# Performance work log

Hardware: AMD Instinct MI355X
Metric: run time of the kernel (lower is better)

## Reference

```python
import jax, jax.numpy as jnp
import numpy as np

N_WIRES = 4
DIM = 16  # 2**4 state-vector length; wire 0 = most significant bit


def _ry(state, theta, wire):
    """Apply RY(theta) on `wire`. state: (N,16) real; theta: (N,) or scalar."""
    s = jnp.moveaxis(state.reshape(-1, 2, 2, 2, 2), 1 + wire, 1)
    c = jnp.cos(theta * 0.5)
    sn = jnp.sin(theta * 0.5)
    if jnp.ndim(theta):
        c = c.reshape(-1, 1, 1, 1)
        sn = sn.reshape(-1, 1, 1, 1)
    s0, s1 = s[:, 0], s[:, 1]
    out = jnp.stack([c * s0 - sn * s1, sn * s0 + c * s1], axis=1)
    return jnp.moveaxis(out, 1, 1 + wire).reshape(-1, DIM)


def _cx_perm(control, target):
    idx = np.arange(DIM)
    cbit = (idx >> (N_WIRES - 1 - control)) & 1
    return np.where(cbit == 1, idx ^ (1 << (N_WIRES - 1 - target)), idx)

# Pauli-Z expectation signs per wire: (16, 4)
_Z_SIGNS = np.stack(
    [1.0 - 2.0 * ((np.arange(DIM) >> (N_WIRES - 1 - w)) & 1) for w in range(N_WIRES)],
    axis=1,
).astype(np.float32)
_CX01 = _cx_perm(0, 1); _CX12 = _cx_perm(1, 2); _CX23 = _cx_perm(2, 3)
_CX02 = _cx_perm(0, 2); _CX13 = _cx_perm(1, 3)


def _init_state(n, dtype):
    return jnp.zeros((n, DIM), dtype).at[:, 0].set(1.0)  # |0000>


def _encode(angles):
    """Fresh device + RY(angle_w) on each wire. angles: (N,4) -> state (N,16)."""
    state = _init_state(angles.shape[0], angles.dtype)
    for w in range(N_WIRES):
        state = _ry(state, angles[:, w], w)
    return state


def _measure_z(state):
    return (state * state) @ jnp.asarray(_Z_SIGNS, state.dtype)  # (N,4)


def _quanv_features(angles, rl_params):
    """Encoder + fixed 8-op 'random layer' (5 RY + 3 CX) + MeasureAll(Z)."""
    s = _encode(angles)
    s = _ry(s, rl_params[0], 0)
    s = _ry(s, rl_params[1], 1)
    s = s[:, _CX02]
    s = _ry(s, rl_params[2], 2)
    s = _ry(s, rl_params[3], 3)
    s = s[:, _CX13]
    s = _ry(s, rl_params[4], 0)
    s = s[:, _CX23]
    return _measure_z(s)  # (N,4)


def _attn_raw(angles):
    """Encoder + CX(0,1),CX(1,2),CX(2,3), measure Z on wire 0."""
    s = _encode(angles)
    s = s[:, _CX01]
    s = s[:, _CX12]
    s = s[:, _CX23]
    return _measure_z(s)[:, 0]  # (N,)


def setup_inputs() -> dict:
    key = jax.random.key(0)
    k1, k2, k3 = jax.random.split(key, 3)
    B = 4096
    x = jax.random.uniform(k1, (B, 784), dtype=jnp.float32)
    rl_params = jax.random.normal(k2, (5,), dtype=jnp.float32)
    W = jax.random.normal(k3, (10, 784), dtype=jnp.float32) * 0.03
    b = jnp.zeros((10,), jnp.float32)
    return {"x": x, "rl_params": rl_params, "W": W, "b": b}


def reference(x, rl_params, W, b):
    B = x.shape[0]
    img = x.reshape(B, 28, 28)
    # 2x2 patches in row-major order -> (B*196, 4) with order [tl, tr, bl, br]
    angles = img.reshape(B, 14, 2, 14, 2).transpose(0, 1, 3, 2, 4).reshape(B * 196, 4)
    feats = _quanv_features(angles, rl_params).reshape(B, 196, 4)
    raw = _attn_raw(feats.reshape(B * 196, 4)).reshape(B, 196)
    attn = jax.nn.softmax(raw, axis=1)
    weighted = (feats * attn[:, :, None]).reshape(B, 4 * 14 * 14)
    logits = weighted @ W.T + b
    return jax.nn.log_softmax(logits, axis=-1)
```

## Files before the change

### kernel.cpp

```cpp
#include <hip/hip_runtime.h>

#define NTHREADS 256
#define NPATCH 196


__device__ __forceinline__ float dot4(float4 a, float4 b) {
    return a.x * b.x + a.y * b.y + a.z * b.z + a.w * b.w;
}

__device__ __forceinline__ float wave_sum63(float x) {
#define DPP_STEP(ctrl, rmask)                                                   \
    x += __int_as_float(__builtin_amdgcn_update_dpp(                            \
        0, __float_as_int(x), (ctrl), (rmask), 0xf, true));
    DPP_STEP(0x111, 0xf)
    DPP_STEP(0x112, 0xf)
    DPP_STEP(0x114, 0xf)
    DPP_STEP(0x118, 0xf)
    DPP_STEP(0x142, 0xa)
    DPP_STEP(0x143, 0xc)
#undef DPP_STEP
    return x;
}

__global__ __launch_bounds__(NTHREADS, 6) void quanv_fused(
    const float* __restrict__ x, const float* __restrict__ rl,
    const float* __restrict__ W, const float* __restrict__ bias,
    float* __restrict__ out)
{
    __shared__ float redw[4];
    __shared__ float redl[4][10];

    const int lane = threadIdx.x & 63;
    const int wave = threadIdx.x >> 6;
    const int il   = wave >> 1;
    const int half = wave & 1;
    const int img  = blockIdx.x * 2 + il;

    const float* __restrict__ xb = x + (size_t)img * 784;

    float srl2, crl2, srl4, crl4;
    __sincosf(rl[2], &srl2, &crl2);
    __sincosf(rl[4], &srl4, &crl4);
    const float rl0 = rl[0], rl1 = rl[1], rl3v = rl[3];

    const int p0 = half * 98 + lane;
    const bool has2 = (lane < 34);
    const int pp1 = has2 ? (p0 + 64) : p0;

    auto patchf = [&](int p, float& f0, float& f1, float& f2, float& f3) {
        const int pi = p / 14;
        const int base = 56 * pi + 2 * (p - pi * 14);
        const float2 top = *reinterpret_cast<const float2*>(xb + base);
        const float2 bot = *reinterpret_cast<const float2*>(xb + base + 28);
        float sa, ca; __sincosf(top.x + rl0, &sa, &ca);
        float s2, c2; __sincosf(bot.x, &s2, &c2);
        f1 = __cosf(top.y + rl1);
        const float cd = __cosf(bot.y + rl3v);
        f0 = crl4 * ca - srl4 * sa * s2;
        f2 = crl2 * ca * c2 - srl2 * s2;
        f3 = f1 * cd * f2;
    };

    float f00, f01, f02, f03; patchf(p0,  f00, f01, f02, f03);
    float f10, f11, f12, f13; patchf(pp1, f10, f11, f12, f13);

    const float e0 = __expf(__cosf(f00));
    const float e1 = has2 ? __expf(__cosf(f10)) : 0.f;

    const float svw = wave_sum63(e0 + e1);
    if (lane == 63) redw[wave] = svw;
    __syncthreads();
    const float inv = 1.0f / (redw[wave & ~1] + redw[wave | 1]);

    const float sc0 = e0 * inv, sc1 = e1 * inv;
    const float4 g0 = make_float4(f00 * sc0, f01 * sc0, f02 * sc0, f03 * sc0);
    const float4 g1 = make_float4(f10 * sc1, f11 * sc1, f12 * sc1, f13 * sc1);

    const float4* __restrict__ W4 = reinterpret_cast<const float4*>(W);
    float acc[10];
    #pragma unroll
    for (int k = 0; k < 10; ++k) {
        acc[k] = dot4(g0, W4[k * NPATCH + p0]) + dot4(g1, W4[k * NPATCH + pp1]);
    }

    #pragma unroll
    for (int k = 0; k < 10; ++k) acc[k] = wave_sum63(acc[k]);
    if (lane == 63) {
        #pragma unroll
        for (int k = 0; k < 10; ++k) redl[wave][k] = acc[k];
    }
    __syncthreads();

    if (half == 0) {
        float lg[10];
        #pragma unroll
        for (int k = 0; k < 10; ++k)
            lg[k] = redl[wave][k] + redl[wave + 1][k] + bias[k];
        float m2 = lg[0];
        #pragma unroll
        for (int k = 1; k < 10; ++k) m2 = fmaxf(m2, lg[k]);
        float ssum = 0.f;
        #pragma unroll
        for (int k = 0; k < 10; ++k) ssum += __expf(lg[k] - m2);
        const float lse = m2 + __logf(ssum);
        if (lane < 10) {
            float myv = lg[0];
            #pragma unroll
            for (int k = 1; k < 10; ++k) myv = (lane == k) ? lg[k] : myv;
            out[(size_t)img * 10 + lane] = myv - lse;
        }
    }
}

extern "C" void kernel_launch(void* const* d_in, const int* in_sizes, int n_in,
                              void* d_out, int out_size, void* d_ws, size_t ws_size,
                              hipStream_t stream) {
    const float* x    = (const float*)d_in[0];
    const float* rl   = (const float*)d_in[1];
    const float* W    = (const float*)d_in[2];
    const float* bias = (const float*)d_in[3];
    float* out = (float*)d_out;
    const int B = in_sizes[0] / 784;
    quanv_fused<<<B / 2, NTHREADS, 0, stream>>>(x, rl, W, bias, out);
}
```

Baseline: 13.12 us.

## Map one image per wave with float4 patch-pair loads and no block sync

Each wavefront now processes a whole image (98 patch-pairs, two per lane) instead of two waves sharing one image. It loads float4 rows so each lane handles two adjacent patches. The cross-wave softmax and logit reductions through shared memory and __syncthreads become in-wave DPP sums broadcast via readlane. The aim is to remove block barriers and LDS traffic and to widen memory accesses, at the cost of more registers per lane and fewer waves in the grid relative to the work.

Result: faster. 12.18 us (-7.1%).

```diff
diff --git a/kernel.cpp b/kernel.cpp
--- a/kernel.cpp
+++ b/kernel.cpp
@@ -1,6 +1,5 @@
 #include <hip/hip_runtime.h>
 
-#define NTHREADS 256
 #define NPATCH 196
 
 
@@ -8,7 +7,7 @@
     return a.x * b.x + a.y * b.y + a.z * b.z + a.w * b.w;
 }
 
-__device__ __forceinline__ float wave_sum63(float x) {
+__device__ __forceinline__ float wave_sum_bcast(float x) {
 #define DPP_STEP(ctrl, rmask)                                                   \
     x += __int_as_float(__builtin_amdgcn_update_dpp(                            \
         0, __float_as_int(x), (ctrl), (rmask), 0xf, true));
@@ -19,22 +18,17 @@
     DPP_STEP(0x142, 0xa)
     DPP_STEP(0x143, 0xc)
 #undef DPP_STEP
-    return x;
+    return __int_as_float(__builtin_amdgcn_readlane(__float_as_int(x), 63));
 }
 
-__global__ __launch_bounds__(NTHREADS, 6) void quanv_fused(
+__global__ __launch_bounds__(256) void quanv_fused(
     const float* __restrict__ x, const float* __restrict__ rl,
     const float* __restrict__ W, const float* __restrict__ bias,
     float* __restrict__ out)
 {
-    __shared__ float redw[4];
-    __shared__ float redl[4][10];
-
     const int lane = threadIdx.x & 63;
     const int wave = threadIdx.x >> 6;
-    const int il   = wave >> 1;
-    const int half = wave & 1;
-    const int img  = blockIdx.x * 2 + il;
+    const int img  = blockIdx.x * 4 + wave;
 
     const float* __restrict__ xb = x + (size_t)img * 784;
 
@@ -43,72 +37,79 @@
     __sincosf(rl[4], &srl4, &crl4);
     const float rl0 = rl[0], rl1 = rl[1], rl3v = rl[3];
 
-    const int p0 = half * 98 + lane;
-    const bool has2 = (lane < 34);
-    const int pp1 = has2 ? (p0 + 64) : p0;
-
-    auto patchf = [&](int p, float& f0, float& f1, float& f2, float& f3) {
-        const int pi = p / 14;
-        const int base = 56 * pi + 2 * (p - pi * 14);
-        const float2 top = *reinterpret_cast<const float2*>(xb + base);
-        const float2 bot = *reinterpret_cast<const float2*>(xb + base + 28);
-        float sa, ca; __sincosf(top.x + rl0, &sa, &ca);
-        float s2, c2; __sincosf(bot.x, &s2, &c2);
-        f1 = __cosf(top.y + rl1);
-        const float cd = __cosf(bot.y + rl3v);
-        f0 = crl4 * ca - srl4 * sa * s2;
-        f2 = crl2 * ca * c2 - srl2 * s2;
-        f3 = f1 * cd * f2;
+    auto pairf = [&](int q, float4& fA, float4& fB, float& eA, float& eB) {
+        const int r = (2 * q) / 14;
+        const int c = (2 * q) - r * 14;
+        const float4 top = *reinterpret_cast<const float4*>(xb + 56 * r + 2 * c);
+        const float4 bot = *reinterpret_cast<const float4*>(xb + 56 * r + 2 * c + 28);
+        {
+            float sa, ca; __sincosf(top.x + rl0, &sa, &ca);
+            float s2, c2; __sincosf(bot.x, &s2, &c2);
+            const float f1 = __cosf(top.y + rl1);
+            const float cd = __cosf(bot.y + rl3v);
+            const float f0 = crl4 * ca - srl4 * sa * s2;
+            const float f2 = crl2 * ca * c2 - srl2 * s2;
+            fA = make_float4(f0, f1, f2, f1 * cd * f2);
+            eA = __expf(__cosf(f0));
+        }
+        {
+            float sa, ca; __sincosf(top.z + rl0, &sa, &ca);
+            float s2, c2; __sincosf(bot.z, &s2, &c2);
+            const float f1 = __cosf(top.w + rl1);
+            const float cd = __cosf(bot.w + rl3v);
+            const float f0 = crl4 * ca - srl4 * sa * s2;
+            const float f2 = crl2 * ca * c2 - srl2 * s2;
+            fB = make_float4(f0, f1, f2, f1 * cd * f2);
+            eB = __expf(__cosf(f0));
+        }
     };
 
-    float f00, f01, f02, f03; patchf(p0,  f00, f01, f02, f03);
-    float f10, f11, f12, f13; patchf(pp1, f10, f11, f12, f13);
+    const bool has2 = (lane < 34);
+    const int q2 = has2 ? (lane + 64) : lane;
 
-    const float e0 = __expf(__cosf(f00));
-    const float e1 = has2 ? __expf(__cosf(f10)) : 0.f;
+    float4 fA0, fB0, fA1, fB1;
+    float eA0, eB0, eA1, eB1;
+    pairf(lane, fA0, fB0, eA0, eB0);
+    pairf(q2,   fA1, fB1, eA1, eB1);
+    if (!has2) { eA1 = 0.f; eB1 = 0.f; }
 
-    const float svw = wave_sum63(e0 + e1);
-    if (lane == 63) redw[wave] = svw;
-    __syncthreads();
-    const float inv = 1.0f / (redw[wave & ~1] + redw[wave | 1]);
+    const float inv = 1.0f / wave_sum_bcast(eA0 + eB0 + eA1 + eB1);
 
-    const float sc0 = e0 * inv, sc1 = e1 * inv;
-    const float4 g0 = make_float4(f00 * sc0, f01 * sc0, f02 * sc0, f03 * sc0);
-    const float4 g1 = make_float4(f10 * sc1, f11 * sc1, f12 * sc1, f13 * sc1);
+    const float wA0 = eA0 * inv, wB0 = eB0 * inv;
+    const float wA1 = eA1 * inv, wB1 = eB1 * inv;
+    const float4 gA0 = make_float4(fA0.x * wA0, fA0.y * wA0, fA0.z * wA0, fA0.w * wA0);
+    const float4 gB0 = make_float4(fB0.x * wB0, fB0.y * wB0, fB0.z * wB0, fB0.w * wB0);
+    const float4 gA1 = make_float4(fA1.x * wA1, fA1.y * wA1, fA1.z * wA1, fA1.w * wA1);
+    const float4 gB1 = make_float4(fB1.x * wB1, fB1.y * wB1, fB1.z * wB1, fB1.w * wB1);
 
     const float4* __restrict__ W4 = reinterpret_cast<const float4*>(W);
     float acc[10];
     #pragma unroll
     for (int k = 0; k < 10; ++k) {
-        acc[k] = dot4(g0, W4[k * NPATCH + p0]) + dot4(g1, W4[k * NPATCH + pp1]);
+        const int kb = k * NPATCH;
+        acc[k] = dot4(gA0, W4[kb + 2 * lane])
+               + dot4(gB0, W4[kb + 2 * lane + 1])
+               + dot4(gA1, W4[kb + 2 * q2])
+               + dot4(gB1, W4[kb + 2 * q2 + 1]);
     }
 
+    float lg[10];
     #pragma unroll
-    for (int k = 0; k < 10; ++k) acc[k] = wave_sum63(acc[k]);
-    if (lane == 63) {
+    for (int k = 0; k < 10; ++k) lg[k] = wave_sum_bcast(acc[k]) + bias[k];
+
+    float m2 = lg[0];
+    #pragma unroll
+    for (int k = 1; k < 10; ++k) m2 = fmaxf(m2, lg[k]);
+    float ssum = 0.f;
+    #pragma unroll
+    for (int k = 0; k < 10; ++k) ssum += __expf(lg[k] - m2);
+    const float lse = m2 + __logf(ssum);
+
+    if (lane < 10) {
+        float myv = lg[0];
         #pragma unroll
-        for (int k = 0; k < 10; ++k) redl[wave][k] = acc[k];
-    }
-    __syncthreads();
-
-    if (half == 0) {
-        float lg[10];
-        #pragma unroll
-        for (int k = 0; k < 10; ++k)
-            lg[k] = redl[wave][k] + redl[wave + 1][k] + bias[k];
-        float m2 = lg[0];
-        #pragma unroll
-        for (int k = 1; k < 10; ++k) m2 = fmaxf(m2, lg[k]);
-        float ssum = 0.f;
-        #pragma unroll
-        for (int k = 0; k < 10; ++k) ssum += __expf(lg[k] - m2);
-        const float lse = m2 + __logf(ssum);
-        if (lane < 10) {
-            float myv = lg[0];
-            #pragma unroll
-            for (int k = 1; k < 10; ++k) myv = (lane == k) ? lg[k] : myv;
-            out[(size_t)img * 10 + lane] = myv - lse;
-        }
+        for (int k = 1; k < 10; ++k) myv = (lane == k) ? lg[k] : myv;
+        out[(size_t)img * 10 + lane] = myv - lse;
     }
 }
 
@@ -121,5 +122,5 @@
     const float* bias = (const float*)d_in[3];
     float* out = (float*)d_out;
     const int B = in_sizes[0] / 784;
-    quanv_fused<<<B / 2, NTHREADS, 0, stream>>>(x, rl, W, bias, out);
+    quanv_fused<<<B / 4, 256, 0, stream>>>(x, rl, W, bias, out);
 }
```
